# Kernel optimization log

Hardware: AMD Instinct MI355X
Metric: run time of the kernel (lower is better)

Reference implementation:

```python
import jax, jax.numpy as jnp
import numpy as np

N = 8192        # total nodes (32 events x 256 hits)
G = 32          # events
K = 15          # knn_graph k
FIN = 4         # n_ftx_in
FOUT = 4        # n_ftx_out
SPACE = 3       # n_ftx_space
LAT = 64        # n_ftx_latent
HID = 2 * LAT   # GIN hidden (n_hidden_nodes)


def _leaky(x):
    return jnp.where(x > 0, x, 0.01 * x)


def setup_inputs() -> dict:
    key = jax.random.key(0)
    ks = jax.random.split(key, 20)

    def p(k, shape, fan_in):
        return (jax.random.normal(k, shape, jnp.float32) / jnp.sqrt(jnp.float32(fan_in)))

    inp = {
        "x": jax.random.normal(ks[0], (N, FIN), jnp.float32),
        "batch": (jnp.arange(N) // (N // G)).astype(jnp.int32),
        "condition": jnp.zeros((G, 1), jnp.float32),
        # space_emb FFN: FIN -> LAT -> LAT
        "W_se1": p(ks[1], (FIN, LAT), FIN), "b_se1": jnp.zeros((LAT,), jnp.float32),
        "W_se2": p(ks[2], (LAT, LAT), LAT), "b_se2": jnp.zeros((LAT,), jnp.float32),
        # GINConv 1 MLP: LAT -> HID -> LAT
        "W_g1a": p(ks[3], (LAT, HID), LAT), "b_g1a": jnp.zeros((HID,), jnp.float32),
        "W_g1b": p(ks[4], (HID, LAT), HID), "b_g1b": jnp.zeros((LAT,), jnp.float32),
        # GINConv 2 MLP
        "W_g2a": p(ks[5], (LAT, HID), LAT), "b_g2a": jnp.zeros((HID,), jnp.float32),
        "W_g2b": p(ks[6], (HID, LAT), HID), "b_g2b": jnp.zeros((LAT,), jnp.float32),
        # out_emb FFN: LAT -> LAT -> FOUT
        "W_oe1": p(ks[7], (LAT, LAT), LAT), "b_oe1": jnp.zeros((LAT,), jnp.float32),
        "W_oe2": p(ks[8], (LAT, FOUT), LAT), "b_oe2": jnp.zeros((FOUT,), jnp.float32),
    }
    return inp


def _knn_graph(pos, batch, k):
    # pairwise squared distances within the same event only; no self-loops
    d = jnp.sum((pos[:, None, :] - pos[None, :, :]) ** 2, axis=-1)  # [N, N]
    ii = jnp.arange(pos.shape[0])
    valid = (batch[:, None] == batch[None, :]) & (ii[:, None] != ii[None, :])
    d = jnp.where(valid, d, jnp.float32(1e30))
    _, nbr = jax.lax.top_k(-d, k)                 # [N, K] nearest neighbor ids
    src = nbr.reshape(-1)                          # neighbor j (source)
    dst = jnp.repeat(ii, k)                        # center i (target)
    return jnp.stack([src, dst])                   # PyG edge_index layout


def _gin(h, src, dst, Wa, ba, Wb, bb):
    # GINConv, eps=0: mlp(x_i + sum_j x_j)
    agg = jax.ops.segment_sum(h[src], dst, num_segments=h.shape[0])
    m = h + agg
    return jnp.maximum(m @ Wa + ba, 0.0) @ Wb + bb


def reference(x, batch, condition,
              W_se1, b_se1, W_se2, b_se2,
              W_g1a, b_g1a, W_g1b, b_g1b,
              W_g2a, b_g2a, W_g2b, b_g2b,
              W_oe1, b_oe1, W_oe2, b_oe2):
    # space_emb FFN
    h = _leaky(x @ W_se1 + b_se1) @ W_se2 + b_se2          # [N, LAT]
    # dynamic knn graph on first SPACE dims of the embedding
    ei = _knn_graph(h[:, :SPACE], batch, K)                 # [2, N*K]
    src, dst = ei[0], ei[1]
    # MPLSeq: 2 GINConv layers with residual skip (cond unused, n_cond=0)
    h = h + _gin(h, src, dst, W_g1a, b_g1a, W_g1b, b_g1b)
    h = h + _gin(h, src, dst, W_g2a, b_g2a, W_g2b, b_g2b)
    # out_emb FFN
    x_emb = _leaky(h @ W_oe1 + b_oe1) @ W_oe2 + b_oe2       # [N, FOUT]
    return (h, x_emb, ei)
```

## Files before the change

### kernel.cpp

```cpp
#include <hip/hip_runtime.h>


#define N_NODES 8192
#define NPE     256
#define KNN     15
#define LAT     64
#define HID     128
#define NK      (N_NODES*KNN)
#define NBLK    512
#define NTHR    512
#define NPB     16
#define NEV     32
#define BPEV    16
#define EI0     (N_NODES*LAT + N_NODES*4)
#define PADM    68
#define PADH    68
#define PADT    136

#define BARA_CNT 0
#define BARA_FLG 4096
#define BARB_CNT 8192
#define BARB_FLG 12288
#define BAR_BYTES 16384

#define OFF_HA  BAR_BYTES
#define OFF_HB  (OFF_HA + N_NODES*LAT*4)
#define OFF_POS (OFF_HB + N_NODES*LAT*4)

typedef unsigned short bf16;
typedef unsigned int   u32;
typedef unsigned long long u64;
typedef short s16x8 __attribute__((ext_vector_type(8)));
typedef float f32x4 __attribute__((ext_vector_type(4)));

__device__ __forceinline__ float bf2f(bf16 s) {
    union { u32 u; float f; } v; v.u = ((u32)s) << 16; return v.f;
}
__device__ __forceinline__ bf16 f2bf(float f) {
    union { float f; u32 u; } v; v.f = f;
    u32 u = v.u + 0x7fffu + ((v.u >> 16) & 1u);
    return (bf16)(u >> 16);
}
__device__ __forceinline__ float ldf(const void* p, int i, int f32) {
    return f32 ? ((const float*)p)[i] : bf2f(((const bf16*)p)[i]);
}
__device__ __forceinline__ void st_coh(float* p, float v) {
    __hip_atomic_store(p, v, __ATOMIC_RELAXED, __HIP_MEMORY_SCOPE_AGENT);
}

union Frag { u32 w[4]; s16x8 v; };

__device__ __forceinline__ u32 cvtpk(float a, float b) {
    u32 r; asm("v_cvt_pk_bf16_f32 %0, %1, %2" : "=v"(r) : "v"(a), "v"(b));
    return r;
}
__device__ __forceinline__ float lo2f(u32 w) { union {u32 u; float f;} v; v.u = w << 16;         return v.f; }
__device__ __forceinline__ float hi2f(u32 w) { union {u32 u; float f;} v; v.u = w & 0xffff0000u; return v.f; }

__device__ __forceinline__ void split8(const float* x, Frag& hi, Frag& lo) {
    #pragma unroll
    for (int i = 0; i < 4; i++) {
        hi.w[i] = cvtpk(x[2*i], x[2*i+1]);
        lo.w[i] = cvtpk(x[2*i]   - lo2f(hi.w[i]),
                        x[2*i+1] - hi2f(hi.w[i]));
    }
}
__device__ __forceinline__ void packA(const float* p, Frag& hi, Frag& lo) {
    float xv[8];
    *(float4*)&xv[0] = *(const float4*)p;
    *(float4*)&xv[4] = *(const float4*)(p + 4);
    split8(xv, hi, lo);
}
__device__ __forceinline__ void loadB_bf(const bf16* p, int stride, Frag& f) {
    #pragma unroll
    for (int i = 0; i < 4; i++)
        f.w[i] = (u32)p[(2*i)*stride] | ((u32)p[(2*i+1)*stride] << 16);
}
__device__ __forceinline__ void loadB_f32(const float* p, int stride, Frag& hi, Frag& lo) {
    float xv[8];
    #pragma unroll
    for (int j = 0; j < 8; j++) xv[j] = p[j*stride];
    split8(xv, hi, lo);
}
__device__ __forceinline__ f32x4 MF(const Frag& a, const Frag& b, f32x4 c) {
    return __builtin_amdgcn_mfma_f32_16x16x32_bf16(a.v, b.v, c, 0, 0, 0);
}

struct KArgs {
    const void* x;
    const void* se1; const void* bse1; const void* se2; const void* bse2;
    const void* g1a; const void* bg1a; const void* g1b; const void* bg1b;
    const void* g2a; const void* bg2a; const void* g2b; const void* bg2b;
    const void* oe1; const void* boe1; const void* oe2; const void* boe2;
    const u32* wdet;
    float* hA; float* hB; float* pos; int* bar;
    void* out;
};

struct Shm {
    union {
        int   red[8];
        float hid[NPB][PADH];
        struct { float x[NPE], y[NPE], z[NPE]; } k;
        float st[NPB*LAT];
    } u;
    float m[NPB*PADM];
    float own[NPB*LAT];
    struct { bf16 hi[NPB*PADT]; bf16 lo[NPB*PADT]; } t;
    float sh[NPB*PADH];
    int   snb[NPB*KNN];
    int   flag;
};

__device__ __forceinline__ void eventbar(int* cnt, int* flg) {
    asm volatile("s_waitcnt vmcnt(0)" ::: "memory");
    __syncthreads();
    if (threadIdx.x == 0) {
        if (__hip_atomic_fetch_add(cnt, 1, __ATOMIC_RELAXED,
                                   __HIP_MEMORY_SCOPE_AGENT) == BPEV - 1) {
            __hip_atomic_store(flg, 1, __ATOMIC_RELAXED,
                               __HIP_MEMORY_SCOPE_AGENT);
        }
        int guard = 0;
        while (__hip_atomic_load(flg, __ATOMIC_RELAXED,
                                 __HIP_MEMORY_SCOPE_AGENT) == 0) {
            __builtin_amdgcn_s_sleep(1);
            if (++guard > (1 << 21)) break;
        }
        __builtin_amdgcn_fence(__ATOMIC_ACQUIRE, "workgroup");
    }
    __syncthreads();
}

template<bool LAST>
__device__ __forceinline__ void gin_layer(Shm& S, int base, int f32,
        const float* __restrict__ hin, float* hout,
        const void* Wa, const void* ba, const void* Wb, const void* bb,
        void* out)
{
    const int tid = threadIdx.x;
    const int lane = tid & 63, wv = tid >> 6;
    const int ln15 = lane & 15, kg = lane >> 4;

    {
        const int n = tid >> 5, sl = tid & 31;
        const float2* h2 = (const float2*)hin;
        const int* nb = &S.snb[n*KNN];
        const float2 o = h2[(size_t)(base + n)*32 + sl];
        *(float2*)&S.own[n*LAT + sl*2] = o;
        float2 vv[KNN];
        #pragma unroll
        for (int k = 0; k < KNN; k++) vv[k] = h2[(size_t)nb[k]*32 + sl];
        float2 mm;
        {
            float s0 = vv[0].x+vv[1].x, s1 = vv[2].x+vv[3].x, s2 = vv[4].x+vv[5].x;
            float s3 = vv[6].x+vv[7].x, s4 = vv[8].x+vv[9].x, s5 = vv[10].x+vv[11].x;
            float s6 = vv[12].x+vv[13].x;
            mm.x = o.x + (((s0+s1)+(s2+s3)) + ((s4+s5)+(s6+vv[14].x)));
        }
        {
            float s0 = vv[0].y+vv[1].y, s1 = vv[2].y+vv[3].y, s2 = vv[4].y+vv[5].y;
            float s3 = vv[6].y+vv[7].y, s4 = vv[8].y+vv[9].y, s5 = vv[10].y+vv[11].y;
            float s6 = vv[12].y+vv[13].y;
            mm.y = o.y + (((s0+s1)+(s2+s3)) + ((s4+s5)+(s6+vv[14].y)));
        }
        *(float2*)&S.m[n*PADM + sl*2] = mm;
        __syncthreads();
    }

    {
        const int u0 = wv * 16;
        const float bias = ldf(ba, u0 + ln15, f32);
        f32x4 acc; acc[0] = bias; acc[1] = bias; acc[2] = bias; acc[3] = bias;
        Frag a0h, a0l, a1h, a1l;
        packA(&S.m[ln15*PADM +  0 + kg*8], a0h, a0l);
        packA(&S.m[ln15*PADM + 32 + kg*8], a1h, a1l);
        if (f32) {
            const float* W = (const float*)Wa;
            Frag b0h, b0l, b1h, b1l;
            loadB_f32(W + ( 0 + kg*8)*HID + u0 + ln15, HID, b0h, b0l);
            loadB_f32(W + (32 + kg*8)*HID + u0 + ln15, HID, b1h, b1l);
            acc = MF(a0h, b0h, acc); acc = MF(a0l, b0h, acc); acc = MF(a0h, b0l, acc);
            acc = MF(a1h, b1h, acc); acc = MF(a1l, b1h, acc); acc = MF(a1h, b1l, acc);
        } else {
            const bf16* W = (const bf16*)Wa;
            Frag b0, b1;
            loadB_bf(W + ( 0 + kg*8)*HID + u0 + ln15, HID, b0);
            loadB_bf(W + (32 + kg*8)*HID + u0 + ln15, HID, b1);
            acc = MF(a0h, b0, acc); acc = MF(a0l, b0, acc);
            acc = MF(a1h, b1, acc); acc = MF(a1l, b1, acc);
        }
        #pragma unroll
        for (int r = 0; r < 4; r++) {
            const int row = kg*4 + r;
            float v = acc[r]; v = v > 0.f ? v : 0.f;
            const bf16 h = f2bf(v);
            S.t.hi[row*PADT + u0 + ln15] = h;
            S.t.lo[row*PADT + u0 + ln15] = f2bf(v - bf2f(h));
        }
    }
    __syncthreads();

    if (wv < 4) {
        const int f0 = wv * 16;
        const float bias = ldf(bb, f0 + ln15, f32);
        f32x4 acc; acc[0] = bias; acc[1] = bias; acc[2] = bias; acc[3] = bias;
        #pragma unroll
        for (int s = 0; s < 4; s++) {
            Frag ah, al;
            ah.v = *(const s16x8*)&S.t.hi[ln15*PADT + s*32 + kg*8];
            al.v = *(const s16x8*)&S.t.lo[ln15*PADT + s*32 + kg*8];
            if (f32) {
                const float* W = (const float*)Wb;
                Frag bh, bl;
                loadB_f32(W + (s*32 + kg*8)*LAT + f0 + ln15, LAT, bh, bl);
                acc = MF(ah, bh, acc); acc = MF(al, bh, acc); acc = MF(ah, bl, acc);
            } else {
                const bf16* W = (const bf16*)Wb;
                Frag b;
                loadB_bf(W + (s*32 + kg*8)*LAT + f0 + ln15, LAT, b);
                acc = MF(ah, b, acc); acc = MF(al, b, acc);
            }
        }
        #pragma unroll
        for (int r = 0; r < 4; r++) {
            const int row = kg*4 + r, f = f0 + ln15, gi = base + row;
            const float o = acc[r] + S.own[row*LAT + f];
            if (!LAST) {
                st_coh(&hout[gi*LAT + f], o);
            } else {
                S.sh[row*PADH + f] = o;
                if (f32) ((float*)out)[gi*LAT + f] = o;
                else     ((bf16*)out)[gi*LAT + f] = f2bf(o);
            }
        }
    }
    __syncthreads();
}

__global__ __launch_bounds__(NTHR, 4) void k_fused(KArgs a)
{
    __shared__ Shm S;
    const int tid = threadIdx.x, blk = blockIdx.x;
    const int lane = tid & 63, wv = tid >> 6;
    const int ln15 = lane & 15, kg = lane >> 4;
    const int ev   = blk & (NEV - 1);
    const int slc  = blk >> 5;
    const int base = ev * NPE + slc * NPB;

    {
        int c = 0;
        for (int i = tid; i < 4096; i += NTHR) {
            const u32 x = a.wdet[i];
            c += ((x >> 7)  & 0xffu) >= 0xC8u;
            c += ((x >> 23) & 0xffu) >= 0xC8u;
        }
        #pragma unroll
        for (int s = 32; s >= 1; s >>= 1) c += __shfl_xor(c, s, 64);
        if (lane == 0) S.u.red[wv] = c;
        __syncthreads();
        if (tid == 0) {
            int t = 0;
            #pragma unroll
            for (int i = 0; i < 8; i++) t += S.u.red[i];
            S.flag = (t > 64) ? 1 : 0;
        }
        __syncthreads();
    }
    const int f32 = S.flag;
    __syncthreads();

    {
        #pragma unroll
        for (int p = 0; p < 2; p++) {
            const int e = tid + p*NTHR, n = e >> 6, f = e & 63, node = base + n;
            float xr[4];
            if (f32) {
                const float4 x4 = ((const float4*)a.x)[node];
                xr[0] = x4.x; xr[1] = x4.y; xr[2] = x4.z; xr[3] = x4.w;
            } else {
                const ushort4 x4 = ((const ushort4*)a.x)[node];
                xr[0] = bf2f(x4.x); xr[1] = bf2f(x4.y);
                xr[2] = bf2f(x4.z); xr[3] = bf2f(x4.w);
            }
            float acc = ldf(a.bse1, f, f32);
            #pragma unroll
            for (int i = 0; i < 4; i++)
                acc = fmaf(xr[i], ldf(a.se1, i*LAT + f, f32), acc);
            acc = acc > 0.f ? acc : 0.01f*acc;
            S.u.hid[n][f] = acc;
        }
        __syncthreads();
        if (wv < 4) {
            const int f0 = wv * 16;
            const float bias = ldf(a.bse2, f0 + ln15, f32);
            f32x4 acc; acc[0] = bias; acc[1] = bias; acc[2] = bias; acc[3] = bias;
            Frag a0h, a0l, a1h, a1l;
            packA(&S.u.hid[ln15][ 0 + kg*8], a0h, a0l);
            packA(&S.u.hid[ln15][32 + kg*8], a1h, a1l);
            if (f32) {
                const float* W = (const float*)a.se2;
                Frag b0h, b0l, b1h, b1l;
                loadB_f32(W + ( 0 + kg*8)*LAT + f0 + ln15, LAT, b0h, b0l);
                loadB_f32(W + (32 + kg*8)*LAT + f0 + ln15, LAT, b1h, b1l);
                acc = MF(a0h, b0h, acc); acc = MF(a0l, b0h, acc); acc = MF(a0h, b0l, acc);
                acc = MF(a1h, b1h, acc); acc = MF(a1l, b1h, acc); acc = MF(a1h, b1l, acc);
            } else {
                const bf16* W = (const bf16*)a.se2;
                Frag b0, b1;
                loadB_bf(W + ( 0 + kg*8)*LAT + f0 + ln15, LAT, b0);
                loadB_bf(W + (32 + kg*8)*LAT + f0 + ln15, LAT, b1);
                acc = MF(a0h, b0, acc); acc = MF(a0l, b0, acc);
                acc = MF(a1h, b1, acc); acc = MF(a1l, b1, acc);
            }
            #pragma unroll
            for (int r = 0; r < 4; r++) {
                const int row = kg*4 + r;
                st_coh(&a.hA[(base + row)*LAT + f0 + ln15], acc[r]);
            }
        } else if (tid - 256 < 48) {
            const int idx = tid - 256, n = idx / 3, f = idx % 3;
            float acc = ldf(a.bse2, f, f32);
            if (f32) {
                const float* W = (const float*)a.se2;
                #pragma unroll 8
                for (int j = 0; j < LAT; j++)
                    acc = fmaf(S.u.hid[n][j], W[j*LAT + f], acc);
            } else {
                const bf16* W = (const bf16*)a.se2;
                #pragma unroll 8
                for (int j = 0; j < LAT; j++)
                    acc = fmaf(S.u.hid[n][j], bf2f(W[j*LAT + f]), acc);
            }
            st_coh(&a.pos[(base + n)*3 + f], acc);
        }
    }
    eventbar(a.bar + (BARA_CNT + ev*128)/4, a.bar + (BARA_FLG + ev*128)/4);

    {
        const int eb = ev * NPE;
        if (tid < NPE) {
            S.u.k.x[tid] = a.pos[(size_t)(eb + tid)*3 + 0];
            S.u.k.y[tid] = a.pos[(size_t)(eb + tid)*3 + 1];
            S.u.k.z[tid] = a.pos[(size_t)(eb + tid)*3 + 2];
        }
        __syncthreads();
        const int n0 = base + wv*2, n1 = n0 + 1;
        const int nl0 = n0 - eb, nl1 = n1 - eb;
        const float px0 = S.u.k.x[nl0], py0 = S.u.k.y[nl0], pz0 = S.u.k.z[nl0];
        const float px1 = S.u.k.x[nl1], py1 = S.u.k.y[nl1], pz1 = S.u.k.z[nl1];
        u64 key0[4], key1[4];
        #pragma unroll
        for (int c = 0; c < 4; c++) {
            const int j = 64*c + lane;
            const float qx = S.u.k.x[j], qy = S.u.k.y[j], qz = S.u.k.z[j];
            {
                const float dx = px0 - qx, dy = py0 - qy, dz = pz0 - qz;
                float dd = __fmul_rn(dx, dx);
                dd = __fadd_rn(dd, __fmul_rn(dy, dy));
                dd = __fadd_rn(dd, __fmul_rn(dz, dz));
                key0[c] = ((u64)__float_as_uint(dd) << 32) | (u32)j;
                if (j == nl0) key0[c] = ~0ull;
            }
            {
                const float dx = px1 - qx, dy = py1 - qy, dz = pz1 - qz;
                float dd = __fmul_rn(dx, dx);
                dd = __fadd_rn(dd, __fmul_rn(dy, dy));
                dd = __fadd_rn(dd, __fmul_rn(dz, dz));
                key1[c] = ((u64)__float_as_uint(dd) << 32) | (u32)j;
                if (j == nl1) key1[c] = ~0ull;
            }
        }
        #define CSWAP(K,A,B) { const u64 x_ = K[A], y_ = K[B]; \
                               K[A] = x_ < y_ ? x_ : y_; K[B] = x_ < y_ ? y_ : x_; }
        CSWAP(key0,0,1) CSWAP(key0,2,3) CSWAP(key0,0,2) CSWAP(key0,1,3) CSWAP(key0,1,2)
        CSWAP(key1,0,1) CSWAP(key1,2,3) CSWAP(key1,0,2) CSWAP(key1,1,3) CSWAP(key1,1,2)
        #undef CSWAP
        int myj0 = 0, myj1 = 0;
        #pragma unroll
        for (int k = 0; k < KNN; k++) {
            u64 m0 = key0[0], m1 = key1[0];
            #pragma unroll
            for (int s = 32; s >= 1; s >>= 1) {
                const u64 o0 = __shfl_xor(m0, s, 64);
                const u64 o1 = __shfl_xor(m1, s, 64);
                m0 = o0 < m0 ? o0 : m0;
                m1 = o1 < m1 ? o1 : m1;
            }
            if (lane == k) { myj0 = (int)(u32)m0; myj1 = (int)(u32)m1; }
            const bool h0 = (key0[0] == m0);
            key0[0] = h0 ? key0[1] : key0[0];
            key0[1] = h0 ? key0[2] : key0[1];
            key0[2] = h0 ? key0[3] : key0[2];
            key0[3] = h0 ? ~0ull   : key0[3];
            const bool h1 = (key1[0] == m1);
            key1[0] = h1 ? key1[1] : key1[0];
            key1[1] = h1 ? key1[2] : key1[1];
            key1[2] = h1 ? key1[3] : key1[2];
            key1[3] = h1 ? ~0ull   : key1[3];
        }
        if (lane < KNN) {
            const int gj0 = eb + myj0, gj1 = eb + myj1;
            S.snb[(n0 - base)*KNN + lane] = gj0;
            S.snb[(n1 - base)*KNN + lane] = gj1;
            if (f32) {
                float* o = (float*)a.out;
                o[EI0 + n0*KNN + lane]      = (float)gj0;
                o[EI0 + NK + n0*KNN + lane] = (float)n0;
                o[EI0 + n1*KNN + lane]      = (float)gj1;
                o[EI0 + NK + n1*KNN + lane] = (float)n1;
            } else {
                bf16* o = (bf16*)a.out;
                o[EI0 + n0*KNN + lane]      = f2bf((float)gj0);
                o[EI0 + NK + n0*KNN + lane] = f2bf((float)n0);
                o[EI0 + n1*KNN + lane]      = f2bf((float)gj1);
                o[EI0 + NK + n1*KNN + lane] = f2bf((float)n1);
            }
        }
        __syncthreads();
    }

    gin_layer<false>(S, base, f32, a.hA, a.hB,
                     a.g1a, a.bg1a, a.g1b, a.bg1b, nullptr);
    eventbar(a.bar + (BARB_CNT + ev*128)/4, a.bar + (BARB_FLG + ev*128)/4);

    gin_layer<true>(S, base, f32, a.hB, nullptr,
                    a.g2a, a.bg2a, a.g2b, a.bg2b, a.out);

    {
        if (wv < 4) {
            const int f0 = wv * 16;
            const float bias = ldf(a.boe1, f0 + ln15, f32);
            f32x4 acc; acc[0] = bias; acc[1] = bias; acc[2] = bias; acc[3] = bias;
            Frag a0h, a0l, a1h, a1l;
            packA(&S.sh[ln15*PADH +  0 + kg*8], a0h, a0l);
            packA(&S.sh[ln15*PADH + 32 + kg*8], a1h, a1l);
            if (f32) {
                const float* W = (const float*)a.oe1;
                Frag b0h, b0l, b1h, b1l;
                loadB_f32(W + ( 0 + kg*8)*LAT + f0 + ln15, LAT, b0h, b0l);
                loadB_f32(W + (32 + kg*8)*LAT + f0 + ln15, LAT, b1h, b1l);
                acc = MF(a0h, b0h, acc); acc = MF(a0l, b0h, acc); acc = MF(a0h, b0l, acc);
                acc = MF(a1h, b1h, acc); acc = MF(a1l, b1h, acc); acc = MF(a1h, b1l, acc);
            } else {
                const bf16* W = (const bf16*)a.oe1;
                Frag b0, b1;
                loadB_bf(W + ( 0 + kg*8)*LAT + f0 + ln15, LAT, b0);
                loadB_bf(W + (32 + kg*8)*LAT + f0 + ln15, LAT, b1);
                acc = MF(a0h, b0, acc); acc = MF(a0l, b0, acc);
                acc = MF(a1h, b1, acc); acc = MF(a1l, b1, acc);
            }
            #pragma unroll
            for (int r = 0; r < 4; r++) {
                const int row = kg*4 + r;
                float v = acc[r];
                v = v > 0.f ? v : 0.01f*v;
                S.u.st[row*LAT + f0 + ln15] = v;
            }
        }
        __syncthreads();
        if (tid < NPB*4) {
            const int n = tid >> 2, ff = tid & 3;
            float acc = ldf(a.boe2, ff, f32);
            for (int j = 0; j < LAT; j++)
                acc = fmaf(S.u.st[n*LAT + j], ldf(a.oe2, j*4 + ff, f32), acc);
            const int xo = N_NODES*LAT + (base + n)*4 + ff;
            if (f32) ((float*)a.out)[xo] = acc;
            else     ((bf16*)a.out)[xo] = f2bf(acc);
        }
    }
}

extern "C" void kernel_launch(void* const* d_in, const int* in_sizes, int n_in,
                              void* d_out, int out_size, void* d_ws, size_t ws_size,
                              hipStream_t stream)
{
    (void)in_sizes; (void)n_in; (void)out_size; (void)ws_size;
    char* ws = (char*)d_ws;

    KArgs a;
    a.x   = d_in[0];
    a.se1 = d_in[3];  a.bse1 = d_in[4];  a.se2 = d_in[5];  a.bse2 = d_in[6];
    a.g1a = d_in[7];  a.bg1a = d_in[8];  a.g1b = d_in[9];  a.bg1b = d_in[10];
    a.g2a = d_in[11]; a.bg2a = d_in[12]; a.g2b = d_in[13]; a.bg2b = d_in[14];
    a.oe1 = d_in[15]; a.boe1 = d_in[16]; a.oe2 = d_in[17]; a.boe2 = d_in[18];
    a.wdet = (const u32*)d_in[7];
    a.hA  = (float*)(ws + OFF_HA);
    a.hB  = (float*)(ws + OFF_HB);
    a.pos = (float*)(ws + OFF_POS);
    a.bar = (int*)ws;
    a.out = d_out;

    hipMemsetAsync(d_ws, 0, BAR_BYTES, stream);
    k_fused<<<dim3(NBLK), dim3(NTHR), 0, stream>>>(a);
}
```

Measured before the change: 131.7 us.

## Prefetch GIN weights before event barriers and keep kNN indices in registers

Loads the first-layer GIN weight fragments and bias into registers before each event barrier, so the global loads overlap the spin-wait instead of following it. kNN neighbour indices are packed as two 16-bit local ids per lane and broadcast with shuffles, which removes the shared-memory neighbour array and one block barrier. Position staging becomes a single interleaved copy, and the output-FFN loop branches on dtype once instead of per element. The cost is extra live registers across the barriers and the GIN call, which could raise register pressure under the 4-blocks-per-CU launch bound.

```diff
diff --git a/kernel.cpp b/kernel.cpp
--- a/kernel.cpp
+++ b/kernel.cpp
@@ -85,6 +85,21 @@
 __device__ __forceinline__ f32x4 MF(const Frag& a, const Frag& b, f32x4 c) {
     return __builtin_amdgcn_mfma_f32_16x16x32_bf16(a.v, b.v, c, 0, 0, 0);
 }
+__device__ __forceinline__ void preWa(const void* Wa, const void* ba, int f32,
+        int ncols, int u0, int ln15, int kg,
+        Frag& b0h, Frag& b0l, Frag& b1h, Frag& b1l, float& bias)
+{
+    bias = ldf(ba, u0 + ln15, f32);
+    if (f32) {
+        const float* W = (const float*)Wa;
+        loadB_f32(W + ( 0 + kg*8)*ncols + u0 + ln15, ncols, b0h, b0l);
+        loadB_f32(W + (32 + kg*8)*ncols + u0 + ln15, ncols, b1h, b1l);
+    } else {
+        const bf16* W = (const bf16*)Wa;
+        loadB_bf(W + ( 0 + kg*8)*ncols + u0 + ln15, ncols, b0h);
+        loadB_bf(W + (32 + kg*8)*ncols + u0 + ln15, ncols, b1h);
+    }
+}
 
 struct KArgs {
     const void* x;
@@ -101,14 +116,13 @@
     union {
         int   red[8];
         float hid[NPB][PADH];
-        struct { float x[NPE], y[NPE], z[NPE]; } k;
+        float kp[NPE*3];
         float st[NPB*LAT];
     } u;
     float m[NPB*PADM];
     float own[NPB*LAT];
     struct { bf16 hi[NPB*PADT]; bf16 lo[NPB*PADT]; } t;
     float sh[NPB*PADH];
-    int   snb[NPB*KNN];
     int   flag;
 };
 
@@ -133,24 +147,29 @@
 }
 
 template<bool LAST>
-__device__ __forceinline__ void gin_layer(Shm& S, int base, int f32,
+__device__ __forceinline__ void gin_layer(Shm& S, int base, int eb, int f32,
+        u32 mypack,
         const float* __restrict__ hin, float* hout,
-        const void* Wa, const void* ba, const void* Wb, const void* bb,
-        void* out)
+        const Frag& pb0h, const Frag& pb0l, const Frag& pb1h, const Frag& pb1l,
+        float pbias,
+        const void* Wb, const void* bb, void* out)
 {
     const int tid = threadIdx.x;
     const int lane = tid & 63, wv = tid >> 6;
     const int ln15 = lane & 15, kg = lane >> 4;
 
     {
-        const int n = tid >> 5, sl = tid & 31;
+        const int n = tid >> 5, sl = tid & 31, half = (tid >> 5) & 1;
         const float2* h2 = (const float2*)hin;
-        const int* nb = &S.snb[n*KNN];
         const float2 o = h2[(size_t)(base + n)*32 + sl];
         *(float2*)&S.own[n*LAT + sl*2] = o;
         float2 vv[KNN];
         #pragma unroll
-        for (int k = 0; k < KNN; k++) vv[k] = h2[(size_t)nb[k]*32 + sl];
+        for (int k = 0; k < KNN; k++) {
+            const u32 p = __shfl(mypack, k, 64);
+            const int nb = eb + (int)((p >> (16*half)) & 0xffffu);
+            vv[k] = h2[(size_t)nb*32 + sl];
+        }
         float2 mm;
         {
             float s0 = vv[0].x+vv[1].x, s1 = vv[2].x+vv[3].x, s2 = vv[4].x+vv[5].x;
@@ -170,25 +189,16 @@
 
     {
         const int u0 = wv * 16;
-        const float bias = ldf(ba, u0 + ln15, f32);
-        f32x4 acc; acc[0] = bias; acc[1] = bias; acc[2] = bias; acc[3] = bias;
+        f32x4 acc; acc[0] = pbias; acc[1] = pbias; acc[2] = pbias; acc[3] = pbias;
         Frag a0h, a0l, a1h, a1l;
         packA(&S.m[ln15*PADM +  0 + kg*8], a0h, a0l);
         packA(&S.m[ln15*PADM + 32 + kg*8], a1h, a1l);
         if (f32) {
-            const float* W = (const float*)Wa;
-            Frag b0h, b0l, b1h, b1l;
-            loadB_f32(W + ( 0 + kg*8)*HID + u0 + ln15, HID, b0h, b0l);
-            loadB_f32(W + (32 + kg*8)*HID + u0 + ln15, HID, b1h, b1l);
-            acc = MF(a0h, b0h, acc); acc = MF(a0l, b0h, acc); acc = MF(a0h, b0l, acc);
-            acc = MF(a1h, b1h, acc); acc = MF(a1l, b1h, acc); acc = MF(a1h, b1l, acc);
+            acc = MF(a0h, pb0h, acc); acc = MF(a0l, pb0h, acc); acc = MF(a0h, pb0l, acc);
+            acc = MF(a1h, pb1h, acc); acc = MF(a1l, pb1h, acc); acc = MF(a1h, pb1l, acc);
         } else {
-            const bf16* W = (const bf16*)Wa;
-            Frag b0, b1;
-            loadB_bf(W + ( 0 + kg*8)*HID + u0 + ln15, HID, b0);
-            loadB_bf(W + (32 + kg*8)*HID + u0 + ln15, HID, b1);
-            acc = MF(a0h, b0, acc); acc = MF(a0l, b0, acc);
-            acc = MF(a1h, b1, acc); acc = MF(a1l, b1, acc);
+            acc = MF(a0h, pb0h, acc); acc = MF(a0l, pb0h, acc);
+            acc = MF(a1h, pb1h, acc); acc = MF(a1l, pb1h, acc);
         }
         #pragma unroll
         for (int r = 0; r < 4; r++) {
@@ -247,6 +257,7 @@
     const int ev   = blk & (NEV - 1);
     const int slc  = blk >> 5;
     const int base = ev * NPE + slc * NPB;
+    const int eb   = ev * NPE;
 
     {
         int c = 0;
@@ -335,25 +346,25 @@
             st_coh(&a.pos[(base + n)*3 + f], acc);
         }
     }
+
+    Frag g1b0h, g1b0l, g1b1h, g1b1l; float g1bias;
+    preWa(a.g1a, a.bg1a, f32, HID, wv*16, ln15, kg,
+          g1b0h, g1b0l, g1b1h, g1b1l, g1bias);
     eventbar(a.bar + (BARA_CNT + ev*128)/4, a.bar + (BARA_FLG + ev*128)/4);
 
+    u32 mypack;
     {
-        const int eb = ev * NPE;
-        if (tid < NPE) {
-            S.u.k.x[tid] = a.pos[(size_t)(eb + tid)*3 + 0];
-            S.u.k.y[tid] = a.pos[(size_t)(eb + tid)*3 + 1];
-            S.u.k.z[tid] = a.pos[(size_t)(eb + tid)*3 + 2];
-        }
+        for (int i = tid; i < NPE*3; i += NTHR) S.u.kp[i] = a.pos[(size_t)eb*3 + i];
         __syncthreads();
         const int n0 = base + wv*2, n1 = n0 + 1;
         const int nl0 = n0 - eb, nl1 = n1 - eb;
-        const float px0 = S.u.k.x[nl0], py0 = S.u.k.y[nl0], pz0 = S.u.k.z[nl0];
-        const float px1 = S.u.k.x[nl1], py1 = S.u.k.y[nl1], pz1 = S.u.k.z[nl1];
+        const float px0 = S.u.kp[nl0*3], py0 = S.u.kp[nl0*3+1], pz0 = S.u.kp[nl0*3+2];
+        const float px1 = S.u.kp[nl1*3], py1 = S.u.kp[nl1*3+1], pz1 = S.u.kp[nl1*3+2];
         u64 key0[4], key1[4];
         #pragma unroll
         for (int c = 0; c < 4; c++) {
             const int j = 64*c + lane;
-            const float qx = S.u.k.x[j], qy = S.u.k.y[j], qz = S.u.k.z[j];
+            const float qx = S.u.kp[j*3], qy = S.u.kp[j*3+1], qz = S.u.kp[j*3+2];
             {
                 const float dx = px0 - qx, dy = py0 - qy, dz = pz0 - qz;
                 float dd = __fmul_rn(dx, dx);
@@ -399,10 +410,9 @@
             key1[2] = h1 ? key1[3] : key1[2];
             key1[3] = h1 ? ~0ull   : key1[3];
         }
+        mypack = (u32)myj0 | ((u32)myj1 << 16);
         if (lane < KNN) {
             const int gj0 = eb + myj0, gj1 = eb + myj1;
-            S.snb[(n0 - base)*KNN + lane] = gj0;
-            S.snb[(n1 - base)*KNN + lane] = gj1;
             if (f32) {
                 float* o = (float*)a.out;
                 o[EI0 + n0*KNN + lane]      = (float)gj0;
@@ -417,15 +427,20 @@
                 o[EI0 + NK + n1*KNN + lane] = f2bf((float)n1);
             }
         }
-        __syncthreads();
-    }
-
-    gin_layer<false>(S, base, f32, a.hA, a.hB,
-                     a.g1a, a.bg1a, a.g1b, a.bg1b, nullptr);
+    }
+
+    gin_layer<false>(S, base, eb, f32, mypack, a.hA, a.hB,
+                     g1b0h, g1b0l, g1b1h, g1b1l, g1bias,
+                     a.g1b, a.bg1b, nullptr);
+
+    Frag g2b0h, g2b0l, g2b1h, g2b1l; float g2bias;
+    preWa(a.g2a, a.bg2a, f32, HID, wv*16, ln15, kg,
+          g2b0h, g2b0l, g2b1h, g2b1l, g2bias);
     eventbar(a.bar + (BARB_CNT + ev*128)/4, a.bar + (BARB_FLG + ev*128)/4);
 
-    gin_layer<true>(S, base, f32, a.hB, nullptr,
-                    a.g2a, a.bg2a, a.g2b, a.bg2b, a.out);
+    gin_layer<true>(S, base, eb, f32, mypack, a.hB, nullptr,
+                    g2b0h, g2b0l, g2b1h, g2b1l, g2bias,
+                    a.g2b, a.bg2b, a.out);
 
     {
         if (wv < 4) {
@@ -461,9 +476,18 @@
         __syncthreads();
         if (tid < NPB*4) {
             const int n = tid >> 2, ff = tid & 3;
-            float acc = ldf(a.boe2, ff, f32);
-            for (int j = 0; j < LAT; j++)
-                acc = fmaf(S.u.st[n*LAT + j], ldf(a.oe2, j*4 + ff, f32), acc);
+            float acc;
+            if (f32) {
+                const float* W = (const float*)a.oe2;
+                acc = ((const float*)a.boe2)[ff];
+                for (int j = 0; j < LAT; j++)
+                    acc = fmaf(S.u.st[n*LAT + j], W[j*4 + ff], acc);
+            } else {
+                const bf16* W = (const bf16*)a.oe2;
+                acc = bf2f(((const bf16*)a.boe2)[ff]);
+                for (int j = 0; j < LAT; j++)
+                    acc = fmaf(S.u.st[n*LAT + j], bf2f(W[j*4 + ff]), acc);
+            }
             const int xo = N_NODES*LAT + (base + n)*4 + ff;
             if (f32) ((float*)a.out)[xo] = acc;
             else     ((bf16*)a.out)[xo] = f2bf(acc);
```

After: 132.7 us. Within noise of the previous version (+0.7%).
